# Optimization experiments

Measured on AMD Instinct MI355X. Metric: run time of the kernel, lower is better.

## Reference

```python
import jax, jax.numpy as jnp
import numpy as np

HID = 256

def lstm_cell(x, h, c, Wih, Whh, bih, bhh):
    # PyTorch LSTM gate order: i, f, g, o
    g = x @ Wih.T + h @ Whh.T + bih + bhh
    i, f, gg, o = jnp.split(g, 4, axis=-1)
    c = jax.nn.sigmoid(f) * c + jax.nn.sigmoid(i) * jnp.tanh(gg)
    h = jax.nn.sigmoid(o) * jnp.tanh(c)
    return h, c

def lstm_seq(x, Wih, Whh, bih, bhh):
    # x: [B, T, D] -> outputs [B, T, H], final (h, c)
    B = x.shape[0]
    h0 = jnp.zeros((B, HID), x.dtype)
    def step(carry, xt):
        h, c = lstm_cell(xt, carry[0], carry[1], Wih, Whh, bih, bhh)
        return (h, c), h
    (h, c), ys = jax.lax.scan(step, (h0, h0), jnp.swapaxes(x, 0, 1))
    return jnp.swapaxes(ys, 0, 1), h, c

def setup_inputs():
    key = jax.random.key(0)
    B, M, H_WIN, NTH, NTW = 512, 16, 25, 64, 64
    SAL = NTH * NTW
    ks = iter(jax.random.split(key, 40))
    def U(shape):
        return jax.random.uniform(next(ks), shape, jnp.float32, -0.0625, 0.0625)
    def lstm_p(pfx, din):
        return {pfx + '_Wih': U((4 * HID, din)), pfx + '_Whh': U((4 * HID, HID)),
                pfx + '_bih': U((4 * HID,)), pfx + '_bhh': U((4 * HID,))}
    inp = {
        'encoder_position_inputs': jax.random.normal(next(ks), (B, M, 3), jnp.float32) * 0.1,
        'encoder_saliency_inputs': jax.random.uniform(next(ks), (B, M, NTH, NTW), jnp.float32),
        'decoder_position_inputs': jax.random.normal(next(ks), (B, 1, 3), jnp.float32) * 0.1,
        'decoder_saliency_inputs': jax.random.uniform(next(ks), (B, H_WIN, NTH, NTW), jnp.float32),
    }
    for pfx, din in [('pe', 3), ('se', SAL), ('fe', 2 * HID), ('pd', 3), ('sd', SAL), ('fd', 2 * HID)]:
        inp.update(lstm_p(pfx, din))
    inp['f2_W'] = U((HID, HID)); inp['f2_b'] = U((HID,))
    inp['out_W'] = U((3, HID)); inp['out_b'] = U((3,))
    return inp

def reference(encoder_position_inputs, encoder_saliency_inputs, decoder_position_inputs, decoder_saliency_inputs,
              pe_Wih, pe_Whh, pe_bih, pe_bhh, se_Wih, se_Whh, se_bih, se_bhh,
              fe_Wih, fe_Whh, fe_bih, fe_bhh, pd_Wih, pd_Whh, pd_bih, pd_bhh,
              sd_Wih, sd_Whh, sd_bih, sd_bhh, fd_Wih, fd_Whh, fd_bih, fd_bhh,
              f2_W, f2_b, out_W, out_b):
    B, M = encoder_position_inputs.shape[:2]
    SAL = encoder_saliency_inputs.shape[2] * encoder_saliency_inputs.shape[3]
    # encoder
    out_pos, h1, c1 = lstm_seq(encoder_position_inputs, pe_Wih, pe_Whh, pe_bih, pe_bhh)
    out_sal, h2, c2 = lstm_seq(encoder_saliency_inputs.reshape(B, M, SAL), se_Wih, se_Whh, se_bih, se_bhh)
    conc_enc = jnp.concatenate([out_sal, out_pos], axis=-1)
    _, hf, cf = lstm_seq(conc_enc, fe_Wih, fe_Whh, fe_bih, fe_bhh)
    # decoder: H_WINDOW single-step recurrence; fuse LSTM restarts from (hf, cf) every step
    dec_sal = decoder_saliency_inputs.reshape(B, -1, SAL)
    def step(carry, sal_t):
        inp, h1, c1, h2, c2 = carry
        h1, c1 = lstm_cell(inp, h1, c1, pd_Wih, pd_Whh, pd_bih, pd_bhh)
        h2, c2 = lstm_cell(sal_t, h2, c2, sd_Wih, sd_Whh, sd_bih, sd_bhh)
        conc = jnp.concatenate([h2, h1], axis=-1)
        hfd, _ = lstm_cell(conc, hf, cf, fd_Wih, fd_Whh, fd_bih, fd_bhh)
        fuse2 = hfd @ f2_W.T + f2_b
        delta = fuse2 @ out_W.T + out_b
        pred = inp + delta  # toPosition: orientation + motion
        return (pred, h1, c1, h2, c2), pred
    init = (decoder_position_inputs[:, 0], h1, c1, h2, c2)
    _, preds = jax.lax.scan(step, init, jnp.swapaxes(dec_sal, 0, 1))
    return jnp.swapaxes(preds, 0, 1)  # [B, H_WINDOW, 3]
```

## Files before the change

kernel.cpp:

```cpp
#include <hip/hip_runtime.h>

#define HID 256
#define BATCH 512
#define MENC 16
#define HWIN 25
#define SALSZ 4096
#define BH (BATCH * HID)

typedef __attribute__((ext_vector_type(8))) short bf16x8;
typedef __attribute__((ext_vector_type(4))) float f32x4;

__device__ __forceinline__ float sigmf(float x) { return 1.0f / (1.0f + __expf(-x)); }
__device__ __forceinline__ ushort f2bf(float f) {
    uint32_t u = __float_as_uint(f);
    return (ushort)((u + 0x7fffu + ((u >> 16) & 1u)) >> 16);
}

#define GLOAD_LDS(gp, lp) \
    __builtin_amdgcn_global_load_lds((const __attribute__((address_space(1))) void*)(gp), \
                                     (__attribute__((address_space(3))) void*)(lp), 16, 0, 0)

__device__ __forceinline__ void st_u64(void* p, unsigned long long v) {
    __hip_atomic_store((unsigned long long*)p, v, __ATOMIC_RELAXED, __HIP_MEMORY_SCOPE_AGENT);
}
// ... 72 lines not shown
        const int row = idx >> 3, u = idx & 7;
        const int su = (u ^ (row & 7)) * 8;
        ra[2 * j + 0] = *(const float4*)(Ag + (size_t)row * lda + su);
        ra[2 * j + 1] = *(const float4*)(Ag + (size_t)row * lda + su + 4);
    }
}
__device__ __forceinline__ void writeA128(const float4 ra[4], ushort* Al, int tid)
{
#pragma unroll
    for (int j = 0; j < 2; ++j) {
        const int idx = j * 512 + tid;
        uint4 v;
        v.x = (uint)f2bf(ra[2 * j].x) | ((uint)f2bf(ra[2 * j].y) << 16);
        v.y = (uint)f2bf(ra[2 * j].z) | ((uint)f2bf(ra[2 * j].w) << 16);
        v.z = (uint)f2bf(ra[2 * j + 1].x) | ((uint)f2bf(ra[2 * j + 1].y) << 16);
        v.w = (uint)f2bf(ra[2 * j + 1].z) | ((uint)f2bf(ra[2 * j + 1].w) << 16);
        *(uint4*)(Al + idx * 8) = v;
    }
}
__device__ __forceinline__ void stageB128(const ushort* Bg, int ldw, ushort* Bl, int tid)
{
#pragma unroll
    for (int j = 0; j < 2; ++j) {
        const int idx = j * 512 + tid;
        const int row = idx >> 3, u = idx & 7;
        const int su = (u ^ (row & 7)) * 8;
        GLOAD_LDS(Bg + (size_t)row * ldw + su, Bl + idx * 8);
    }
}

__device__ __forceinline__ void gemm128f_body(
    const float* __restrict__ A, const ushort* __restrict__ W, float* __restrict__ C,
    int lda, int ldw, int ldc, int K, int gx, int nwg, int bid,
    ushort* AsB, ushort* BsB, int tid)
{
    const int lane = tid & 63, wid = tid >> 6;
    {
        const int q = nwg >> 3, r = nwg & 7;
        const int xcd = bid & 7, o = bid >> 3;
        bid = (xcd < r) ? xcd * (q + 1) + o : r * (q + 1) + (xcd - r) * q + o;
    }
    const int m0 = (bid / gx) * 128, n0 = (bid % gx) * 128;

    const int wr = wid >> 1, wc = wid & 1;
    const int fr = lane & 15, fq = lane >> 4;

    f32x4 acc[2][4] = {};
    const int nt = K / 64;
    const float*  Ab0 = A + (size_t)m0 * lda;
    const ushort* Bb0 = W + (size_t)n0 * ldw;

    float4 ra[4];
    loadA128(Ab0, lda, tid, ra);
    stageB128(Bb0, ldw, BsB, tid);
    writeA128(ra, AsB, tid);
    loadA128(Ab0 + 64, lda, tid, ra);
    asm volatile("s_waitcnt vmcnt(4) lgkmcnt(0)" ::: "memory");
    __builtin_amdgcn_sched_barrier(0);
    __builtin_amdgcn_s_barrier();
    __builtin_amdgcn_sched_barrier(0);

    for (int t = 0; t < nt; ++t) {
        const int p = t & 1;
        const int t1 = (t + 1 < nt) ? t + 1 : nt - 1;
        const int t2 = (t + 2 < nt) ? t + 2 : nt - 1;
        stageB128(Bb0 + t1 * 64, ldw, BsB + (p ^ 1) * 8192, tid);
// ... 8 lines not shown
#pragma unroll
            for (int nf = 0; nf < 4; ++nf) {
                const int row = wc * 64 + nf * 16 + fr;
                bfr[nf] = *(const bf16x8*)(Bb + row * 64 + ((ks * 4 + fq) ^ (row & 7)) * 8);
            }
            bf16x8 af[2];
#pragma unroll
            for (int mf = 0; mf < 2; ++mf) {
                const int row = wr * 32 + mf * 16 + fr;
                af[mf] = *(const bf16x8*)(Ab + row * 64 + ((ks * 4 + fq) ^ (row & 7)) * 8);
            }
            __builtin_amdgcn_s_setprio(1);
#pragma unroll
            for (int mf = 0; mf < 2; ++mf)
#pragma unroll
                for (int nf = 0; nf < 4; ++nf)
                    acc[mf][nf] = __builtin_amdgcn_mfma_f32_16x16x32_bf16(
                        af[mf], bfr[nf], acc[mf][nf], 0, 0, 0);
            __builtin_amdgcn_s_setprio(0);
        }
        if (t == nt - 1) break;
        asm volatile("s_waitcnt vmcnt(4) lgkmcnt(0)" ::: "memory");
        __builtin_amdgcn_sched_barrier(0);
        __builtin_amdgcn_s_barrier();
        __builtin_amdgcn_sched_barrier(0);
    }

    const int cl = lane & 15, ch = lane >> 4;
#pragma unroll
    for (int mf = 0; mf < 2; ++mf)
#pragma unroll
        for (int nf = 0; nf < 4; ++nf)
#pragma unroll
            for (int r = 0; r < 4; ++r)
                C[(size_t)(m0 + wr * 32 + mf * 16 + ch * 4 + r) * ldc
                  + n0 + wc * 64 + nf * 16 + cl] = acc[mf][nf][r];
}

__global__ __launch_bounds__(512, 4)
void gemm128f(const float* __restrict__ A, const ushort* __restrict__ W,
              float* __restrict__ C, int gx, int nwg)
{
    __shared__ ushort As[2 * 128 * 64];
    __shared__ ushort Bs[2 * 128 * 64];
    gemm128f_body(A, W, C, SALSZ, SALSZ, 1024, SALSZ, gx, nwg, blockIdx.x, As, Bs, threadIdx.x);
}

__device__ __forceinline__ void gemm128b_body(
    const ushort* __restrict__ A, const ushort* __restrict__ W, float* __restrict__ C,
    int lda, int ldw, int ldc, int K, int gx, int nwg, int bid,
    unsigned int* wflag, unsigned int wcnt, unsigned int* sflag, bool wt,
    ushort* AsB, ushort* BsB, int tid)
{
    const int lane = tid & 63, wid = tid >> 6;
    {
        const int q = nwg >> 3, r = nwg & 7;
        const int xcd = bid & 7, o = bid >> 3;
        bid = (xcd < r) ? xcd * (q + 1) + o : r * (q + 1) + (xcd - r) * q + o;
    }
    const int m0 = (bid / gx) * 128, n0 = (bid % gx) * 128;

    if (wflag) gbar_wait(wflag + (m0 >> 9), wcnt);

    const int wr = wid >> 1, wc = wid & 1;
    const int fr = lane & 15, fq = lane >> 4;

    f32x4 acc[2][4] = {};
    const int nt = K / 64;
    const ushort* Ab0 = A + (size_t)m0 * lda;
    const ushort* Bb0 = W + (size_t)n0 * ldw;

    stageB128(Ab0, lda, AsB, tid);
    stageB128(Bb0, ldw, BsB, tid);
    __syncthreads();

    for (int t = 0; t < nt; ++t) {
        const int p = t & 1;
        if (t + 1 < nt) {
            stageB128(Ab0 + (t + 1) * 64, lda, AsB + (p ^ 1) * 8192, tid);
            stageB128(Bb0 + (t + 1) * 64, ldw, BsB + (p ^ 1) * 8192, tid);
        }
        const ushort* Ab = AsB + p * 8192;
        const ushort* Bb = BsB + p * 8192;
#pragma unroll
        for (int ks = 0; ks < 2; ++ks) {
            bf16x8 bfr[4];
#pragma unroll
            for (int nf = 0; nf < 4; ++nf) {
                const int row = wc * 64 + nf * 16 + fr;
                bfr[nf] = *(const bf16x8*)(Bb + row * 64 + ((ks * 4 + fq) ^ (row & 7)) * 8);
            }
            bf16x8 af[2];
#pragma unroll
            for (int mf = 0; mf < 2; ++mf) {
                const int row = wr * 32 + mf * 16 + fr;
                af[mf] = *(const bf16x8*)(Ab + row * 64 + ((ks * 4 + fq) ^ (row & 7)) * 8);
            }
#pragma unroll
            for (int mf = 0; mf < 2; ++mf)
#pragma unroll
                for (int nf = 0; nf < 4; ++nf)
                    acc[mf][nf] = __builtin_amdgcn_mfma_f32_16x16x32_bf16(
                        af[mf], bfr[nf], acc[mf][nf], 0, 0, 0);
        }
        if (t == nt - 1) break;
        __syncthreads();
    }

    const int cl = lane & 15, ch = lane >> 4;
#pragma unroll
    for (int mf = 0; mf < 2; ++mf)
#pragma unroll
        for (int nf = 0; nf < 4; ++nf)
#pragma unroll
            for (int r = 0; r < 4; ++r) {
                const int mm = m0 + wr * 32 + mf * 16 + ch * 4 + r;
                const int nn = n0 + wc * 64 + nf * 16 + cl;
                if (wt) st_f32(C + (size_t)mm * ldc + nn, acc[mf][nf][r]);
                else    C[(size_t)mm * ldc + nn] = acc[mf][nf][r];
            }
    if (sflag) {
        __syncthreads();
        if (tid == 0) atomicAdd(sflag + (m0 >> 9), 1u);
    }
}

struct EncArgs {
    const ushort *WHse, *WHpe;
    const float  *xg_se;
    const float  *enc_pos;
    const float  *se_b1, *se_b2, *pe_b1, *pe_b2;
    const float  *pe_Wih;
    ushort       *conc;
    float        *SE_C, *PE_C;
    unsigned int *bar;
};

__global__ __launch_bounds__(512, 4)
void enc_sd(EncArgs A, const float* __restrict__ sdA, const ushort* __restrict__ sdW,
            float* __restrict__ sdC)
{
    __shared__ ushort sh[34816];
    const int tid = threadIdx.x;

    if (blockIdx.x >= 128) {
        gemm128f_body(sdA, sdW, sdC, SALSZ, SALSZ, 1024, SALSZ, 8, 800,
                      (int)blockIdx.x - 128, sh, sh + 16384, tid);
        return;
    }

    const int lane = tid & 63, w = tid >> 6;
    const int role  = blockIdx.x >> 6;
    const int rem   = blockIdx.x & 63;
    const int btile = rem & 7, usup = rem >> 3;
    const int b0 = btile * 64, ub = usup * 32;
    const int usub = w & 1, bsub = w >> 1;
    const int u0t = ub + usub * 16;
    const int grp = role * 8 + btile;
    const int fr = lane & 15, fq = lane >> 4;
    const int u = u0t + fr;
    const int ul = usub * 16 + fr;
    const int coff = role ? 256 : 0;
    ushort* Ws0 = sh + usub * 16384;
    ushort (*hloc)[32] = (ushort(*)[32])(sh + 32768);

    stage_wtile(role ? A.WHpe : A.WHse, HID, u0t, Ws0, lane, bsub);

    const float* b1 = role ? A.pe_b1 : A.se_b1;
    const float* b2 = role ? A.pe_b2 : A.se_b2;
    float bias[4], wxs[4][3];
#pragma unroll
    for (int g = 0; g < 4; ++g) {
        bias[g] = b1[g * HID + u] + b2[g * HID + u];
        wxs[g][0] = wxs[g][1] = wxs[g][2] = 0.0f;
        if (role) {
            wxs[g][0] = A.pe_Wih[(g * HID + u) * 3 + 0];
            wxs[g][1] = A.pe_Wih[(g * HID + u) * 3 + 1];
            wxs[g][2] = A.pe_Wih[(g * HID + u) * 3 + 2];
        }
    }
    float c[4] = {0.f, 0.f, 0.f, 0.f};
    __syncthreads();

    for (int t = 0; t < MENC; ++t) {
        float xg[4][4];
#pragma unroll
        for (int r = 0; r < 4; ++r) {
            const int b = b0 + bsub * 16 + fq * 4 + r;
            if (role) {
                const float* xp = A.enc_pos + ((size_t)b * MENC + t) * 3;
                xg[r][0] = xp[0]; xg[r][1] = xp[1]; xg[r][2] = xp[2]; xg[r][3] = 0.f;
            } else {
#pragma unroll
                for (int g = 0; g < 4; ++g)
                    xg[r][g] = A.xg_se[((size_t)b * MENC + t) * 1024 + g * HID + u];
            }
        }
        if (t > 0) gbar_wait(A.bar + grp * MENC + (t - 1), 8);
        f32x4 acc[4] = {};
        if (t > 0)
            cell_g(A.conc + ((size_t)(t - 1) * 512 + b0 + bsub * 16) * 512 + coff, 512,
                   Ws0, acc, lane);
#pragma unroll
        for (int r = 0; r < 4; ++r) {
            const int bl = bsub * 16 + fq * 4 + r;
            const int b = b0 + bl;
            float gv[4];
#pragma unroll
            for (int g = 0; g < 4; ++g) {
                float v = acc[g][r] + bias[g];
                if (role) v += xg[r][0] * wxs[g][0] + xg[r][1] * wxs[g][1] + xg[r][2] * wxs[g][2];
                else      v += xg[r][g];
                gv[g] = v;
            }
            const float cn = sigmf(gv[1]) * c[r] + sigmf(gv[0]) * tanhf(gv[2]);
            const float hn = sigmf(gv[3]) * tanhf(cn);
            c[r] = cn;
            hloc[bl][ul] = f2bf(hn);
            if (t == MENC - 1) (role ? A.PE_C : A.SE_C)[(size_t)b * HID + u] = cn;
        }
        __syncthreads();
        {
            const int row = tid >> 3, c8 = tid & 7;
            const unsigned long long v = *(const unsigned long long*)&hloc[row][c8 * 4];
            st_u64(A.conc + ((size_t)t * 512 + b0 + row) * 512 + coff + ub + c8 * 4, v);
        }
        if (t != MENC - 1) gbar_arrive(A.bar + grp * MENC + t);
    }
}

struct MidArgs {
    const ushort *WHsd, *WHfe;
    const float  *xg_sd;
    const float  *xg_fe;
    const float  *sd_b1, *sd_b2, *fe_b1, *fe_b2;
    const ushort *conc;
    const float  *SE_C;
    ushort       *SDB;
    ushort       *FEB;
    float        *FEH, *FE_C;
    unsigned int *bar;
    unsigned int *fe_done;
    unsigned int *sdb_done;
};

__global__ __launch_bounds__(512, 4)
void mid_fe_xh2(MidArgs A, const ushort* __restrict__ feA, const ushort* __restrict__ feW,
                float* __restrict__ feC,
                const ushort* __restrict__ xA, const ushort* __restrict__ xW,
                float* __restrict__ xC)
{
    __shared__ ushort sh[34816];
    const int tid = threadIdx.x;

    if (blockIdx.x >= 640) {
        gemm128b_body(xA, xW, xC, 256, 512, 1024, 256, 8, 800,
                      (int)blockIdx.x - 640, A.sdb_done, 64, nullptr, false,
                      sh, sh + 16384, tid);
        return;
    }
    if (blockIdx.x >= 128) {
        gemm128b_body(feA, feW, feC, 512, 512, 1024, 512, 8, 512,
                      (int)blockIdx.x - 128, nullptr, 0, A.fe_done, true,
                      sh, sh + 16384, tid);
        return;
    }

    const int lane = tid & 63, w = tid >> 6;
    const int role  = blockIdx.x >> 6;
    const int rem   = blockIdx.x & 63;
    const int btile = rem & 7, usup = rem >> 3;
    const int b0 = btile * 64, ub = usup * 32;
    const int usub = w & 1, bsub = w >> 1;
    const int u0t = ub + usub * 16;
    const int grp = role * 8 + btile;
    const int fr = lane & 15, fq = lane >> 4;
    const int u = u0t + fr;
    const int ul = usub * 16 + fr;
    const int NT = role ? MENC : HWIN;
    ushort* Ws0 = sh + usub * 16384;
    ushort (*hloc)[32] = (ushort(*)[32])(sh + 32768);

    stage_wtile(role ? A.WHfe : A.WHsd, HID, u0t, Ws0, lane, bsub);

    const float* b1 = role ? A.fe_b1 : A.sd_b1;
    const float* b2 = role ? A.fe_b2 : A.sd_b2;
    float bias[4];
#pragma unroll
    for (int g = 0; g < 4; ++g) bias[g] = b1[g * HID + u] + b2[g * HID + u];

    float c[4];
#pragma unroll
    for (int r = 0; r < 4; ++r) {
        const int b = b0 + bsub * 16 + fq * 4 + r;
        c[r] = role ? 0.0f : A.SE_C[(size_t)b * HID + u];
    }
    __syncthreads();

    for (int t = 0; t < NT; ++t) {
        if (role) gbar_wait(A.fe_done + t, 32);
        float xg[4][4];
#pragma unroll
        for (int r = 0; r < 4; ++r) {
            const int b = b0 + bsub * 16 + fq * 4 + r;
#pragma unroll
            for (int g = 0; g < 4; ++g)
                xg[r][g] = role ? A.xg_fe[((size_t)t * 512 + b) * 1024 + g * HID + u]
                                : A.xg_sd[((size_t)b * HWIN + t) * 1024 + g * HID + u];
        }
        if (t > 0) gbar_wait(A.bar + grp * HWIN + (t - 1), 8);
        f32x4 acc[4] = {};
        if (role == 0) {
            if (t == 0) cell_g(A.conc + ((size_t)15 * 512 + b0 + bsub * 16) * 512, 512,
                               Ws0, acc, lane);
            else        cell_g(A.SDB + ((size_t)(t - 1) * 512 + b0 + bsub * 16) * HID, HID,
                               Ws0, acc, lane);
        } else if (t > 0) {
            cell_g(A.FEB + ((size_t)(t - 1) * BATCH + b0 + bsub * 16) * HID, HID,
                   Ws0, acc, lane);
        }
#pragma unroll
        for (int r = 0; r < 4; ++r) {
            const int bl = bsub * 16 + fq * 4 + r;
            const int b = b0 + bl;
            float gv[4];
#pragma unroll
            for (int g = 0; g < 4; ++g)
                gv[g] = acc[g][r] + bias[g] + xg[r][g];
            const float cn = sigmf(gv[1]) * c[r] + sigmf(gv[0]) * tanhf(gv[2]);
            const float hn = sigmf(gv[3]) * tanhf(cn);
            c[r] = cn;
            hloc[bl][ul] = f2bf(hn);
            if (role == 1 && t == MENC - 1) {
                A.FEH[(size_t)b * HID + u] = hn;
                A.FE_C[(size_t)b * HID + u] = cn;
            }
        }
        __syncthreads();
        {
            const int row = tid >> 3, c8 = tid & 7;
            const unsigned long long v = *(const unsigned long long*)&hloc[row][c8 * 4];
            ushort* dst = role ? (A.FEB + ((size_t)t * BATCH + b0 + row) * 256 + ub + c8 * 4)
                               : (A.SDB + ((size_t)t * 512 + b0 + row) * 256 + ub + c8 * 4);
            st_u64(dst, v);
        }
        __syncthreads();
        if (tid == 0) {
            if (role == 0) atomicAdd(A.sdb_done + t, 1u);
            if (t != NT - 1) atomicAdd(A.bar + grp * HWIN + t, 1u);
        }
    }
}

__global__ __launch_bounds__(256)
void gemm_tn(const float* __restrict__ A, const float* __restrict__ W,
             const float* __restrict__ b1, const float* __restrict__ b2,
             float* __restrict__ C,
             int M, int N, int K, int lda, int ldw, int ldc)
{
    __shared__ float AsT[16][68];
    __shared__ float WsT[16][68];
    const int t  = threadIdx.x;
    const int tx = t & 15, ty = t >> 4;
    const int m0 = blockIdx.y * 64, n0 = blockIdx.x * 64;
    const int lr = t >> 2;
    const int c4 = t & 3;

    float acc[4][4];
#pragma unroll
    for (int i = 0; i < 4; ++i)
#pragma unroll
        for (int j = 0; j < 4; ++j) acc[i][j] = 0.0f;

    for (int k0 = 0; k0 < K; k0 += 16) {
        float a[4], w[4];
        const int kb = k0 + c4 * 4;
#pragma unroll
        for (int k = 0; k < 4; ++k) {
            a[k] = (kb + k < K) ? A[(size_t)(m0 + lr) * lda + kb + k] : 0.0f;
            w[k] = (kb + k < K) ? W[(size_t)(n0 + lr) * ldw + kb + k] : 0.0f;
        }
        __syncthreads();
#pragma unroll
        for (int k = 0; k < 4; ++k) {
            AsT[c4 * 4 + k][lr] = a[k];
            WsT[c4 * 4 + k][lr] = w[k];
        }
        __syncthreads();
#pragma unroll
        for (int kk = 0; kk < 16; ++kk) {
            const float4 av = *(const float4*)&AsT[kk][ty * 4];
            const float4 wv = *(const float4*)&WsT[kk][tx * 4];
            acc[0][0] += av.x * wv.x; acc[0][1] += av.x * wv.y; acc[0][2] += av.x * wv.z; acc[0][3] += av.x * wv.w;
            acc[1][0] += av.y * wv.x; acc[1][1] += av.y * wv.y; acc[1][2] += av.y * wv.z; acc[1][3] += av.y * wv.w;
            acc[2][0] += av.z * wv.x; acc[2][1] += av.z * wv.y; acc[2][2] += av.z * wv.z; acc[2][3] += av.z * wv.w;
            acc[3][0] += av.w * wv.x; acc[3][1] += av.w * wv.y; acc[3][2] += av.w * wv.z; acc[3][3] += av.w * wv.w;
        }
    }

#pragma unroll
    for (int i = 0; i < 4; ++i) {
        const int m = m0 + ty * 4 + i;
#pragma unroll
        for (int j = 0; j < 4; ++j) {
            const int n = n0 + tx * 4 + j;
            float v = acc[i][j];
            if (b1) v += b1[n];
            if (b2) v += b2[n];
            C[(size_t)m * ldc + n] = v;
        }
    }
}

struct DecArgs {
    const ushort *WHpd;
    const ushort *WFDh;
    const ushort *peF;
    const float  *PE_C, *FE_C, *GBIAS;
    const float  *xh2;
    const float  *pd_b1, *pd_b2, *pd_Wih;
    const float  *G, *c3, *dec_pos;
    ushort       *H1;
    float        *DELTA;
    float        *out;
    unsigned int *bar;
};

__global__ __launch_bounds__(512)
void dec_chain(DecArgs A)
{
    __shared__ ushort Wpd[2][64 * 256], Wfd[2][64 * 256];
    __shared__ ushort hloc[64][32];
    __shared__ float pred_lds[192];
    const int tid = threadIdx.x, lane = tid & 63, w = tid >> 6;
    const int btile = blockIdx.x & 7, usup = blockIdx.x >> 3;
    const int b0 = btile * 64, ub = usup * 32;
    const int usub = w & 1, bsub = w >> 1;
    const int u0t = ub + usub * 16;
    const int fr = lane & 15, fq = lane >> 4;
    const int u = u0t + fr;
    const int ul = usub * 16 + fr;
    unsigned int* bars = A.bar + btile * 2 * HWIN;

    stage_wtile(A.WHpd, HID, u0t, Wpd[usub], lane, bsub);
    stage_wtile(A.WFDh, 512, u0t, Wfd[usub], lane, bsub);

    float pdb[4], wxs[4][3], cf[4], c1[4], Gu[3], gb[4][4];
#pragma unroll
    for (int g = 0; g < 4; ++g) {
        pdb[g] = A.pd_b1[g * HID + u] + A.pd_b2[g * HID + u];
        wxs[g][0] = A.pd_Wih[(g * HID + u) * 3 + 0];
        wxs[g][1] = A.pd_Wih[(g * HID + u) * 3 + 1];
        wxs[g][2] = A.pd_Wih[(g * HID + u) * 3 + 2];
    }
#pragma unroll
    for (int r = 0; r < 4; ++r) {
        const int b = b0 + bsub * 16 + fq * 4 + r;
        c1[r] = A.PE_C[(size_t)b * HID + u];
        cf[r] = A.FE_C[(size_t)b * HID + u];
#pragma unroll
        for (int g = 0; g < 4; ++g) gb[r][g] = A.GBIAS[(size_t)b * 1024 + g * HID + u];
    }
    Gu[0] = A.G[0 * HID + u]; Gu[1] = A.G[1 * HID + u]; Gu[2] = A.G[2 * HID + u];
    const float c3r = (tid < 192) ? A.c3[tid % 3] : 0.0f;
    if (tid < 192) pred_lds[tid] = A.dec_pos[(size_t)(b0 + tid / 3) * 3 + tid % 3];
    __syncthreads();

    for (int t = 0; t < HWIN; ++t) {
        f32x4 acc[4] = {};
        if (t == 0) cell_g(A.peF + (size_t)(b0 + bsub * 16) * 512, 512, Wpd[usub], acc, lane);
        else        cell_g(A.H1 + ((size_t)(t - 1) * BATCH + b0 + bsub * 16) * HID, HID,
                           Wpd[usub], acc, lane);
        if (t > 0) {
            gbar_wait(bars + 2 * (t - 1) + 1, 8);
            if (tid < 192) {
                pred_lds[tid] += A.DELTA[((size_t)(t - 1) * 512 + b0 + tid / 3) * 3 + tid % 3] + c3r;
                if (usup == 0)
                    A.out[((size_t)(b0 + tid / 3) * HWIN + (t - 1)) * 3 + tid % 3] = pred_lds[tid];
            }
            __syncthreads();
        }
#pragma unroll
        for (int r = 0; r < 4; ++r) {
            const int bl = bsub * 16 + fq * 4 + r;
            const float x0 = pred_lds[bl * 3 + 0];
            const float x1 = pred_lds[bl * 3 + 1];
            const float x2 = pred_lds[bl * 3 + 2];
            float gv[4];
#pragma unroll
            for (int g = 0; g < 4; ++g)
                gv[g] = acc[g][r] + pdb[g] + x0 * wxs[g][0] + x1 * wxs[g][1] + x2 * wxs[g][2];
            const float cn = sigmf(gv[1]) * c1[r] + sigmf(gv[0]) * tanhf(gv[2]);
            const float hn = sigmf(gv[3]) * tanhf(cn);
            c1[r] = cn;
            hloc[bl][ul] = f2bf(hn);
        }
        __syncthreads();
        {
            const int row = tid >> 3, c8 = tid & 7;
            const unsigned long long v = *(const unsigned long long*)&hloc[row][c8 * 4];
            st_u64(A.H1 + ((size_t)t * BATCH + b0 + row) * 256 + ub + c8 * 4, v);
        }
        gbar_arrive(bars + 2 * t);
        float xh[4][4];
#pragma unroll
        for (int r = 0; r < 4; ++r) {
            const int b = b0 + bsub * 16 + fq * 4 + r;
#pragma unroll
            for (int g = 0; g < 4; ++g)
                xh[r][g] = A.xh2[((size_t)t * 512 + b) * 1024 + g * HID + u];
        }
        gbar_wait(bars + 2 * t, 8);
        {
            f32x4 accB[4] = {};
            cell_g(A.H1 + ((size_t)t * BATCH + b0 + bsub * 16) * HID, HID,
                   Wfd[usub], accB, lane);
#pragma unroll
            for (int r = 0; r < 4; ++r) {
                const int b = b0 + bsub * 16 + fq * 4 + r;
                float gv[4];
#pragma unroll
                for (int g = 0; g < 4; ++g)
                    gv[g] = accB[g][r] + xh[r][g] + gb[r][g];
                const float cn = sigmf(gv[1]) * cf[r] + sigmf(gv[0]) * tanhf(gv[2]);
                const float hn = sigmf(gv[3]) * tanhf(cn);
                float p0 = hn * Gu[0], p1 = hn * Gu[1], p2 = hn * Gu[2];
#pragma unroll
                for (int s = 1; s < 16; s <<= 1) {
                    p0 += __shfl_xor(p0, s);
                    p1 += __shfl_xor(p1, s);
                    p2 += __shfl_xor(p2, s);
                }
                if (fr == 0) {
                    float* d = A.DELTA + ((size_t)t * 512 + b) * 3;
                    atomicAdd(d + 0, p0); atomicAdd(d + 1, p1); atomicAdd(d + 2, p2);
                }
            }
        }
        gbar_arrive(bars + 2 * t + 1);
    }
    gbar_wait(bars + 2 * (HWIN - 1) + 1, 8);
    if (tid < 192) {
        pred_lds[tid] += A.DELTA[((size_t)(HWIN - 1) * 512 + b0 + tid / 3) * 3 + tid % 3] + c3r;
        if (usup == 0)
            A.out[((size_t)(b0 + tid / 3) * HWIN + (HWIN - 1)) * 3 + tid % 3] = pred_lds[tid];
    }
}

__global__ __launch_bounds__(256)
void precompute_G(const float* __restrict__ f2W, const float* __restrict__ f2b,
                  const float* __restrict__ outW, const float* __restrict__ outb,
                  float* __restrict__ G, float* __restrict__ c3)
{
    const int k = threadIdx.x;
    float g0 = 0.f, g1 = 0.f, g2 = 0.f;
    for (int n = 0; n < HID; ++n) {
        const float w = f2W[n * HID + k];
        g0 += outW[n] * w;
        g1 += outW[HID + n] * w;
        g2 += outW[2 * HID + n] * w;
    }
    G[k] = g0; G[HID + k] = g1; G[2 * HID + k] = g2;
    if (k < 3) {
        float s = outb[k];
        for (int n = 0; n < HID; ++n) s += outW[k * HID + n] * f2b[n];
        c3[k] = s;
    }
}

extern "C" void kernel_launch(void* const* d_in, const int* in_sizes, int n_in,
                              void* d_out, int out_size, void* d_ws, size_t ws_size,
                              hipStream_t stream)
{
    (void)in_sizes; (void)n_in; (void)out_size; (void)ws_size;
    const float* enc_pos = (const float*)d_in[0];
    const float* enc_sal = (const float*)d_in[1];
    const float* dec_pos = (const float*)d_in[2];
    const float* dec_sal = (const float*)d_in[3];
// ... 14 lines not shown
    float* out = (float*)d_out;
    float* ws  = (float*)d_ws;

    size_t off = 0;
    float* XG_SE = ws + off; off += (size_t)8192 * 1024;
    float* XG_FE = ws + off; off += (size_t)8192 * 1024;
    float* BIG   = ws + off; off += (size_t)12800 * 1024;
    float* BIG2  = ws + off; off += (size_t)12800 * 1024;
    float* GBIAS = ws + off; off += (size_t)BATCH * 1024;
    float* PE_C  = ws + off; off += BH;
    float* SE_C  = ws + off; off += BH;
    float* FE_C  = ws + off; off += BH;
    float* FEH   = ws + off; off += BH;
    float* Gm    = ws + off; off += 1024;
    float* C3    = ws + off; off += 8;
    float* DELTA = ws + off; off += (size_t)HWIN * BATCH * 3 + 64;
    unsigned int* BAR = (unsigned int*)(ws + off); off += 1280;
    ushort* WSE  = (ushort*)(ws + off); off += ((size_t)1024 * 4096) / 2;
    ushort* WSD  = (ushort*)(ws + off); off += ((size_t)1024 * 4096) / 2;
    ushort* WFE  = (ushort*)(ws + off); off += ((size_t)1024 * 512) / 2;
    ushort* WFD  = (ushort*)(ws + off); off += ((size_t)1024 * 512) / 2;
    ushort* WHpe = (ushort*)(ws + off); off += ((size_t)1024 * 256) / 2;
    ushort* WHse = (ushort*)(ws + off); off += ((size_t)1024 * 256) / 2;
    ushort* WHfe = (ushort*)(ws + off); off += ((size_t)1024 * 256) / 2;
    ushort* WHsd = (ushort*)(ws + off); off += ((size_t)1024 * 256) / 2;
    ushort* WHpd = (ushort*)(ws + off); off += ((size_t)1024 * 256) / 2;
    ushort* CONC = (ushort*)(ws + off); off += ((size_t)MENC * 512 * 512) / 2;
    ushort* SDB  = (ushort*)(ws + off); off += ((size_t)HWIN * BH) / 2;
    ushort* FEB  = (ushort*)(ws + off); off += ((size_t)MENC * BH) / 2;
    ushort* H1   = (ushort*)(ws + off); off += ((size_t)HWIN * BH) / 2;

    unsigned int* FE_DONE  = BAR + 1100;
    unsigned int* SDB_DONE = BAR + 1160;

    hipMemsetAsync(DELTA, 0, ((size_t)HWIN * BATCH * 3 + 64 + 1280) * 4, stream);

    {
        Cvt9 a;
        const float* srcs[9] = { se_Wih, sd_Wih, fe_Wih, fd_Wih, pe_Whh, se_Whh, fe_Whh, sd_Whh, pd_Whh };
        ushort*      dsts[9] = { WSE,    WSD,    WFE,    WFD,    WHpe,   WHse,   WHfe,   WHsd,   WHpd };
        const int    n4s[9]  = { 1024*4096/4, 1024*4096/4, 1024*512/4, 1024*512/4,
                                 1024*256/4, 1024*256/4, 1024*256/4, 1024*256/4, 1024*256/4 };
        int acc9 = 0;
        for (int i = 0; i < 9; ++i) { a.s[i] = srcs[i]; a.d[i] = dsts[i]; acc9 += n4s[i]; a.end[i] = acc9; }
        cvt_multi<<<(acc9 + 255) / 256, 256, 0, stream>>>(a);
    }
    precompute_G<<<1, 256, 0, stream>>>(f2_W, f2_b, out_W, out_b, Gm, C3);

    gemm128f<<<512, 512, 0, stream>>>(enc_sal, WSE, XG_SE, 8, 512);

    {
        EncArgs a;
        a.WHse = WHse; a.WHpe = WHpe; a.xg_se = XG_SE; a.enc_pos = enc_pos;
        a.se_b1 = se_bih; a.se_b2 = se_bhh; a.pe_b1 = pe_bih; a.pe_b2 = pe_bhh;
        a.pe_Wih = pe_Wih; a.conc = CONC; a.SE_C = SE_C; a.PE_C = PE_C;
        a.bar = BAR;
        enc_sd<<<928, 512, 0, stream>>>(a, dec_sal, WSD, BIG);
    }

    {
        MidArgs a;
        a.WHsd = WHsd; a.WHfe = WHfe; a.xg_sd = BIG; a.xg_fe = XG_FE;
        a.sd_b1 = sd_bih; a.sd_b2 = sd_bhh; a.fe_b1 = fe_bih; a.fe_b2 = fe_bhh;
        a.conc = CONC; a.SE_C = SE_C; a.SDB = SDB; a.FEB = FEB;
        a.FEH = FEH; a.FE_C = FE_C; a.bar = BAR + 256;
        a.fe_done = FE_DONE; a.sdb_done = SDB_DONE;
        mid_fe_xh2<<<1440, 512, 0, stream>>>(a, CONC, WFE, XG_FE, SDB, WFD, BIG2);
    }

    gemm_tn<<<dim3(16, 8), 256, 0, stream>>>(FEH, fd_Whh, fd_bih, fd_bhh, GBIAS,
                                             BATCH, 1024, HID, HID, HID, 1024);

    {
        DecArgs a;
        a.WHpd = WHpd; a.WFDh = WFD + 256;
        a.peF = CONC + ((size_t)15 * 512) * 512 + 256;
        a.PE_C = PE_C; a.FE_C = FE_C; a.GBIAS = GBIAS; a.xh2 = BIG2;
        a.pd_b1 = pd_bih; a.pd_b2 = pd_bhh; a.pd_Wih = pd_Wih;
        a.G = Gm; a.c3 = C3; a.dec_pos = dec_pos;
        a.H1 = H1; a.DELTA = DELTA; a.out = out; a.bar = BAR + 656;
        dec_chain<<<64, 512, 0, stream>>>(a);
    }
}
```

Measured before the change: 957.1 us.

## Merge mid-stage, bias GEMM and decoder chain into one persistent kernel

Folds the fd_Whh bias GEMM and the decoder recurrence into the mid-stage kernel as extra block roles, synchronised with global flag counters. The decoder can then start as soon as its inputs are ready instead of waiting at kernel boundaries. The xh2 GEMM now adds GBIAS in its epilogue, which removes the per-step bias add in the decoder. The decoder is re-tiled to 128-batch by 16-unit blocks. This removes two launches and lets the work overlap, but it relies on spin-wait barriers that assume all blocks are co-resident, and it changes the decoder's tile shape.

```diff
diff --git a/kernel.cpp b/kernel.cpp
--- a/kernel.cpp
+++ b/kernel.cpp
@@ -220,6 +220,7 @@
     const ushort* __restrict__ A, const ushort* __restrict__ W, float* __restrict__ C,
     int lda, int ldw, int ldc, int K, int gx, int nwg, int bid,
     unsigned int* wflag, unsigned int wcnt, unsigned int* sflag, bool wt,
+    const float* __restrict__ rbias,
     ushort* AsB, ushort* BsB, int tid)
 {
     const int lane = tid & 63, wid = tid >> 6;
@@ -286,8 +287,10 @@
             for (int r = 0; r < 4; ++r) {
                 const int mm = m0 + wr * 32 + mf * 16 + ch * 4 + r;
                 const int nn = n0 + wc * 64 + nf * 16 + cl;
-                if (wt) st_f32(C + (size_t)mm * ldc + nn, acc[mf][nf][r]);
-                else    C[(size_t)mm * ldc + nn] = acc[mf][nf][r];
+                float v = acc[mf][nf][r];
+                if (rbias) v += rbias[(size_t)(mm & 511) * ldc + nn];
+                if (wt) st_f32(C + (size_t)mm * ldc + nn, v);
+                else    C[(size_t)mm * ldc + nn] = v;
             }
     if (sflag) {
         __syncthreads();
@@ -399,10 +402,9 @@
     }
 }
 
-struct MidArgs {
+struct P3Args {
     const ushort *WHsd, *WHfe;
-    const float  *xg_sd;
-    const float  *xg_fe;
+    const float  *xg_sd, *xg_fe;
     const float  *sd_b1, *sd_b2, *fe_b1, *fe_b2;
     const ushort *conc;
     const float  *SE_C;
@@ -412,33 +414,208 @@
     unsigned int *bar;
     unsigned int *fe_done;
     unsigned int *sdb_done;
+    const ushort *feW;
+    float        *feC;
+    const float  *fd_Whh, *fd_b1, *fd_b2;
+    float        *GBIAS;
+    unsigned int *fe_fin;
+    unsigned int *gb_done;
+    const ushort *xW;
+    float        *xh2C;
+    unsigned int *xh2_done;
+    const ushort *WHpd, *WFDh, *peF;
+    const float  *PE_C;
+    const float  *pd_b1, *pd_b2, *pd_Wih;
+    const float  *G, *c3, *dec_pos;
+    ushort       *H1;
+    float        *DELTA;
+    float        *out;
+    unsigned int *dbar;
 };
 
+__device__ __forceinline__ void tn_body(const P3Args& A, int idx, ushort* shm, int tid)
+{
+    gbar_wait(A.fe_fin, 64);
+    float* As = (float*)shm;
+    float* Ws = As + 16 * 68;
+    const int m0 = (idx >> 4) * 64, n0 = (idx & 15) * 64;
+    const int lr = tid >> 3, kc = tid & 7;
+    const int tx = tid & 15, ty = tid >> 4;
+    float acc[2][4] = {};
+    for (int k0 = 0; k0 < HID; k0 += 16) {
+        const float a0 = A.FEH[(size_t)(m0 + lr) * HID + k0 + kc * 2];
+        const float a1 = A.FEH[(size_t)(m0 + lr) * HID + k0 + kc * 2 + 1];
+        const float w0 = A.fd_Whh[(size_t)(n0 + lr) * HID + k0 + kc * 2];
+        const float w1 = A.fd_Whh[(size_t)(n0 + lr) * HID + k0 + kc * 2 + 1];
+        __syncthreads();
+        As[(kc * 2) * 68 + lr] = a0; As[(kc * 2 + 1) * 68 + lr] = a1;
+        Ws[(kc * 2) * 68 + lr] = w0; Ws[(kc * 2 + 1) * 68 + lr] = w1;
+        __syncthreads();
+#pragma unroll
+        for (int kk = 0; kk < 16; ++kk) {
+            const float av0 = As[kk * 68 + ty * 2], av1 = As[kk * 68 + ty * 2 + 1];
+            const float4 wv = *(const float4*)&Ws[kk * 68 + tx * 4];
+            acc[0][0] += av0 * wv.x; acc[0][1] += av0 * wv.y; acc[0][2] += av0 * wv.z; acc[0][3] += av0 * wv.w;
+            acc[1][0] += av1 * wv.x; acc[1][1] += av1 * wv.y; acc[1][2] += av1 * wv.z; acc[1][3] += av1 * wv.w;
+        }
+    }
+#pragma unroll
+    for (int i = 0; i < 2; ++i) {
+        const int m = m0 + ty * 2 + i;
+#pragma unroll
+        for (int j = 0; j < 4; ++j) {
+            const int n = n0 + tx * 4 + j;
+            st_f32(A.GBIAS + (size_t)m * 1024 + n, acc[i][j] + A.fd_b1[n] + A.fd_b2[n]);
+        }
+    }
+    __syncthreads();
+    if (tid == 0) atomicAdd(A.gb_done, 1u);
+}
+
+__device__ __forceinline__ void dec_body(const P3Args& A, int idx, ushort* shm, int tid)
+{
+    ushort* Wpd = shm;
+    ushort* Wfd = shm + 16384;
+    ushort (*hloc)[16] = (ushort(*)[16])(shm + 32768);
+    float* pred_lds = (float*)(shm + 34816);
+    const int lane = tid & 63, w = tid >> 6;
+    const int btile = idx & 3, usup = idx >> 2;
+    const int b0 = btile * 128, u0t = usup * 16;
+    const int bsub = w;
+    const int fr = lane & 15, fq = lane >> 4;
+    const int u = u0t + fr;
+    unsigned int* bars = A.dbar + btile * 2 * HWIN;
+
+    if (w < 4) stage_wtile(A.WHpd, HID, u0t, Wpd, lane, w);
+    else       stage_wtile(A.WFDh, 512, u0t, Wfd, lane, w - 4);
+
+    float pdb[4], wxs[4][3], cf[4], c1[4], Gu[3];
+#pragma unroll
+    for (int g = 0; g < 4; ++g) {
+        pdb[g] = A.pd_b1[g * HID + u] + A.pd_b2[g * HID + u];
+        wxs[g][0] = A.pd_Wih[(g * HID + u) * 3 + 0];
+        wxs[g][1] = A.pd_Wih[(g * HID + u) * 3 + 1];
+        wxs[g][2] = A.pd_Wih[(g * HID + u) * 3 + 2];
+    }
+#pragma unroll
+    for (int r = 0; r < 4; ++r)
+        c1[r] = A.PE_C[(size_t)(b0 + bsub * 16 + fq * 4 + r) * HID + u];
+    Gu[0] = A.G[u]; Gu[1] = A.G[HID + u]; Gu[2] = A.G[2 * HID + u];
+    const float c3r = (tid < 384) ? A.c3[tid % 3] : 0.0f;
+    if (tid < 384) pred_lds[tid] = A.dec_pos[(size_t)(b0 + tid / 3) * 3 + tid % 3];
+
+    gbar_wait(A.gb_done, 128);
+#pragma unroll
+    for (int r = 0; r < 4; ++r)
+        cf[r] = A.FE_C[(size_t)(b0 + bsub * 16 + fq * 4 + r) * HID + u];
+
+    for (int t = 0; t < HWIN; ++t) {
+        f32x4 acc[4] = {};
+        if (t == 0) cell_g(A.peF + (size_t)(b0 + bsub * 16) * 512, 512, Wpd, acc, lane);
+        else        cell_g(A.H1 + ((size_t)(t - 1) * BATCH + b0 + bsub * 16) * HID, HID,
+                           Wpd, acc, lane);
+        if (t > 0) {
+            gbar_wait(bars + 2 * (t - 1) + 1, 16);
+            if (tid < 384) {
+                pred_lds[tid] += A.DELTA[((size_t)(t - 1) * 512 + b0 + tid / 3) * 3 + tid % 3] + c3r;
+                if (usup == 0)
+                    A.out[((size_t)(b0 + tid / 3) * HWIN + (t - 1)) * 3 + tid % 3] = pred_lds[tid];
+            }
+            __syncthreads();
+        }
+#pragma unroll
+        for (int r = 0; r < 4; ++r) {
+            const int bl = bsub * 16 + fq * 4 + r;
+            const float x0 = pred_lds[bl * 3 + 0];
+            const float x1 = pred_lds[bl * 3 + 1];
+            const float x2 = pred_lds[bl * 3 + 2];
+            float gv[4];
+#pragma unroll
+            for (int g = 0; g < 4; ++g)
+                gv[g] = acc[g][r] + pdb[g] + x0 * wxs[g][0] + x1 * wxs[g][1] + x2 * wxs[g][2];
+            const float cn = sigmf(gv[1]) * c1[r] + sigmf(gv[0]) * tanhf(gv[2]);
+            const float hn = sigmf(gv[3]) * tanhf(cn);
+            c1[r] = cn;
+            hloc[bl][fr] = f2bf(hn);
+        }
+        __syncthreads();
+        {
+            const int row = tid >> 2, c4 = tid & 3;
+            const unsigned long long v = *(const unsigned long long*)&hloc[row][c4 * 4];
+            st_u64(A.H1 + ((size_t)t * BATCH + b0 + row) * 256 + u0t + c4 * 4, v);
+        }
+        gbar_arrive(bars + 2 * t);
+        gbar_wait(A.xh2_done + t, 32);
+        float xh[4][4];
+#pragma unroll
+        for (int r = 0; r < 4; ++r) {
+            const int b = b0 + bsub * 16 + fq * 4 + r;
+#pragma unroll
+            for (int g = 0; g < 4; ++g)
+                xh[r][g] = A.xh2C[((size_t)t * 512 + b) * 1024 + g * HID + u];
+        }
+        gbar_wait(bars + 2 * t, 16);
+        {
+            f32x4 accB[4] = {};
+            cell_g(A.H1 + ((size_t)t * BATCH + b0 + bsub * 16) * HID, HID, Wfd, accB, lane);
+#pragma unroll
+            for (int r = 0; r < 4; ++r) {
+                const int b = b0 + bsub * 16 + fq * 4 + r;
+                float gv[4];
+#pragma unroll
+                for (int g = 0; g < 4; ++g)
+                    gv[g] = accB[g][r] + xh[r][g];
+                const float cn = sigmf(gv[1]) * cf[r] + sigmf(gv[0]) * tanhf(gv[2]);
+                const float hn = sigmf(gv[3]) * tanhf(cn);
+                float p0 = hn * Gu[0], p1 = hn * Gu[1], p2 = hn * Gu[2];
+#pragma unroll
+                for (int s = 1; s < 16; s <<= 1) {
+                    p0 += __shfl_xor(p0, s);
+                    p1 += __shfl_xor(p1, s);
+                    p2 += __shfl_xor(p2, s);
+                }
+                if (fr == 0) {
+                    float* d = A.DELTA + ((size_t)t * 512 + b) * 3;
+                    atomicAdd(d + 0, p0); atomicAdd(d + 1, p1); atomicAdd(d + 2, p2);
+                }
+            }
+        }
+        gbar_arrive(bars + 2 * t + 1);
+    }
+    gbar_wait(bars + 2 * (HWIN - 1) + 1, 16);
+    if (tid < 384) {
+        pred_lds[tid] += A.DELTA[((size_t)(HWIN - 1) * 512 + b0 + tid / 3) * 3 + tid % 3] + c3r;
+        if (usup == 0)
+            A.out[((size_t)(b0 + tid / 3) * HWIN + (HWIN - 1)) * 3 + tid % 3] = pred_lds[tid];
+    }
+}
+
 __global__ __launch_bounds__(512, 4)
-void mid_fe_xh2(MidArgs A, const ushort* __restrict__ feA, const ushort* __restrict__ feW,
-                float* __restrict__ feC,
-                const ushort* __restrict__ xA, const ushort* __restrict__ xW,
-                float* __restrict__ xC)
-{
-    __shared__ ushort sh[34816];
+void mid_dec(P3Args A)
+{
+    __shared__ ushort sh[35584];
     const int tid = threadIdx.x;
-
-    if (blockIdx.x >= 640) {
-        gemm128b_body(xA, xW, xC, 256, 512, 1024, 256, 8, 800,
-                      (int)blockIdx.x - 640, A.sdb_done, 64, nullptr, false,
+    const int blk = (int)blockIdx.x;
+
+    if (blk >= 832) {
+        gbar_wait(A.gb_done, 128);
+        gemm128b_body(A.SDB, A.xW, A.xh2C, 256, 512, 1024, 256, 8, 800,
+                      blk - 832, A.sdb_done, 64, A.xh2_done, true, A.GBIAS,
                       sh, sh + 16384, tid);
         return;
     }
-    if (blockIdx.x >= 128) {
-        gemm128b_body(feA, feW, feC, 512, 512, 1024, 512, 8, 512,
-                      (int)blockIdx.x - 128, nullptr, 0, A.fe_done, true,
+    if (blk >= 768) { dec_body(A, blk - 768, sh, tid); return; }
+    if (blk >= 640) { tn_body(A, blk - 640, sh, tid); return; }
+    if (blk >= 128) {
+        gemm128b_body(A.conc, A.feW, A.feC, 512, 512, 1024, 512, 8, 512,
+                      blk - 128, nullptr, 0, A.fe_done, true, nullptr,
                       sh, sh + 16384, tid);
         return;
     }
 
     const int lane = tid & 63, w = tid >> 6;
-    const int role  = blockIdx.x >> 6;
-    const int rem   = blockIdx.x & 63;
+    const int role  = blk >> 6;
+    const int rem   = blk & 63;
     const int btile = rem & 7, usup = rem >> 3;
     const int b0 = btile * 64, ub = usup * 32;
     const int usub = w & 1, bsub = w >> 1;
@@ -502,8 +679,8 @@
             c[r] = cn;
             hloc[bl][ul] = f2bf(hn);
             if (role == 1 && t == MENC - 1) {
-                A.FEH[(size_t)b * HID + u] = hn;
-                A.FE_C[(size_t)b * HID + u] = cn;
+                st_f32(A.FEH + (size_t)b * HID + u, hn);
+                st_f32(A.FE_C + (size_t)b * HID + u, cn);
             }
         }
         __syncthreads();
@@ -520,200 +697,8 @@
             if (t != NT - 1) atomicAdd(A.bar + grp * HWIN + t, 1u);
         }
     }
-}
-
-__global__ __launch_bounds__(256)
-void gemm_tn(const float* __restrict__ A, const float* __restrict__ W,
-             const float* __restrict__ b1, const float* __restrict__ b2,
-             float* __restrict__ C,
-             int M, int N, int K, int lda, int ldw, int ldc)
-{
-    __shared__ float AsT[16][68];
-    __shared__ float WsT[16][68];
-    const int t  = threadIdx.x;
-    const int tx = t & 15, ty = t >> 4;
-    const int m0 = blockIdx.y * 64, n0 = blockIdx.x * 64;
-    const int lr = t >> 2;
-    const int c4 = t & 3;
-
-    float acc[4][4];
-#pragma unroll
-    for (int i = 0; i < 4; ++i)
-#pragma unroll
-        for (int j = 0; j < 4; ++j) acc[i][j] = 0.0f;
-
-    for (int k0 = 0; k0 < K; k0 += 16) {
-        float a[4], w[4];
-        const int kb = k0 + c4 * 4;
-#pragma unroll
-        for (int k = 0; k < 4; ++k) {
-            a[k] = (kb + k < K) ? A[(size_t)(m0 + lr) * lda + kb + k] : 0.0f;
-            w[k] = (kb + k < K) ? W[(size_t)(n0 + lr) * ldw + kb + k] : 0.0f;
-        }
-        __syncthreads();
-#pragma unroll
-        for (int k = 0; k < 4; ++k) {
-            AsT[c4 * 4 + k][lr] = a[k];
-            WsT[c4 * 4 + k][lr] = w[k];
-        }
-        __syncthreads();
-#pragma unroll
-        for (int kk = 0; kk < 16; ++kk) {
-            const float4 av = *(const float4*)&AsT[kk][ty * 4];
-            const float4 wv = *(const float4*)&WsT[kk][tx * 4];
-            acc[0][0] += av.x * wv.x; acc[0][1] += av.x * wv.y; acc[0][2] += av.x * wv.z; acc[0][3] += av.x * wv.w;
-            acc[1][0] += av.y * wv.x; acc[1][1] += av.y * wv.y; acc[1][2] += av.y * wv.z; acc[1][3] += av.y * wv.w;
-            acc[2][0] += av.z * wv.x; acc[2][1] += av.z * wv.y; acc[2][2] += av.z * wv.z; acc[2][3] += av.z * wv.w;
-            acc[3][0] += av.w * wv.x; acc[3][1] += av.w * wv.y; acc[3][2] += av.w * wv.z; acc[3][3] += av.w * wv.w;
-        }
-    }
-
-#pragma unroll
-    for (int i = 0; i < 4; ++i) {
-        const int m = m0 + ty * 4 + i;
-#pragma unroll
-        for (int j = 0; j < 4; ++j) {
-            const int n = n0 + tx * 4 + j;
-            float v = acc[i][j];
-            if (b1) v += b1[n];
-            if (b2) v += b2[n];
-            C[(size_t)m * ldc + n] = v;
-        }
-    }
-}
-
-struct DecArgs {
-    const ushort *WHpd;
-    const ushort *WFDh;
-    const ushort *peF;
-    const float  *PE_C, *FE_C, *GBIAS;
-    const float  *xh2;
-    const float  *pd_b1, *pd_b2, *pd_Wih;
-    const float  *G, *c3, *dec_pos;
-    ushort       *H1;
-    float        *DELTA;
-    float        *out;
-    unsigned int *bar;
-};
-
-__global__ __launch_bounds__(512)
-void dec_chain(DecArgs A)
-{
-    __shared__ ushort Wpd[2][64 * 256], Wfd[2][64 * 256];
-    __shared__ ushort hloc[64][32];
-    __shared__ float pred_lds[192];
-    const int tid = threadIdx.x, lane = tid & 63, w = tid >> 6;
-    const int btile = blockIdx.x & 7, usup = blockIdx.x >> 3;
-    const int b0 = btile * 64, ub = usup * 32;
-    const int usub = w & 1, bsub = w >> 1;
-    const int u0t = ub + usub * 16;
-    const int fr = lane & 15, fq = lane >> 4;
-    const int u = u0t + fr;
-    const int ul = usub * 16 + fr;
-    unsigned int* bars = A.bar + btile * 2 * HWIN;
-
-    stage_wtile(A.WHpd, HID, u0t, Wpd[usub], lane, bsub);
-    stage_wtile(A.WFDh, 512, u0t, Wfd[usub], lane, bsub);
-
-    float pdb[4], wxs[4][3], cf[4], c1[4], Gu[3], gb[4][4];
-#pragma unroll
-    for (int g = 0; g < 4; ++g) {
-        pdb[g] = A.pd_b1[g * HID + u] + A.pd_b2[g * HID + u];
-        wxs[g][0] = A.pd_Wih[(g * HID + u) * 3 + 0];
-        wxs[g][1] = A.pd_Wih[(g * HID + u) * 3 + 1];
-        wxs[g][2] = A.pd_Wih[(g * HID + u) * 3 + 2];
-    }
-#pragma unroll
-    for (int r = 0; r < 4; ++r) {
-        const int b = b0 + bsub * 16 + fq * 4 + r;
-        c1[r] = A.PE_C[(size_t)b * HID + u];
-        cf[r] = A.FE_C[(size_t)b * HID + u];
-#pragma unroll
-        for (int g = 0; g < 4; ++g) gb[r][g] = A.GBIAS[(size_t)b * 1024 + g * HID + u];
-    }
-    Gu[0] = A.G[0 * HID + u]; Gu[1] = A.G[1 * HID + u]; Gu[2] = A.G[2 * HID + u];
-    const float c3r = (tid < 192) ? A.c3[tid % 3] : 0.0f;
-    if (tid < 192) pred_lds[tid] = A.dec_pos[(size_t)(b0 + tid / 3) * 3 + tid % 3];
-    __syncthreads();
-
-    for (int t = 0; t < HWIN; ++t) {
-        f32x4 acc[4] = {};
-        if (t == 0) cell_g(A.peF + (size_t)(b0 + bsub * 16) * 512, 512, Wpd[usub], acc, lane);
-        else        cell_g(A.H1 + ((size_t)(t - 1) * BATCH + b0 + bsub * 16) * HID, HID,
-                           Wpd[usub], acc, lane);
-        if (t > 0) {
-            gbar_wait(bars + 2 * (t - 1) + 1, 8);
-            if (tid < 192) {
-                pred_lds[tid] += A.DELTA[((size_t)(t - 1) * 512 + b0 + tid / 3) * 3 + tid % 3] + c3r;
-                if (usup == 0)
-                    A.out[((size_t)(b0 + tid / 3) * HWIN + (t - 1)) * 3 + tid % 3] = pred_lds[tid];
-            }
-            __syncthreads();
-        }
-#pragma unroll
-        for (int r = 0; r < 4; ++r) {
-            const int bl = bsub * 16 + fq * 4 + r;
-            const float x0 = pred_lds[bl * 3 + 0];
-            const float x1 = pred_lds[bl * 3 + 1];
-            const float x2 = pred_lds[bl * 3 + 2];
-            float gv[4];
-#pragma unroll
-            for (int g = 0; g < 4; ++g)
-                gv[g] = acc[g][r] + pdb[g] + x0 * wxs[g][0] + x1 * wxs[g][1] + x2 * wxs[g][2];
-            const float cn = sigmf(gv[1]) * c1[r] + sigmf(gv[0]) * tanhf(gv[2]);
-            const float hn = sigmf(gv[3]) * tanhf(cn);
-            c1[r] = cn;
-            hloc[bl][ul] = f2bf(hn);
-        }
-        __syncthreads();
-        {
-            const int row = tid >> 3, c8 = tid & 7;
-            const unsigned long long v = *(const unsigned long long*)&hloc[row][c8 * 4];
-            st_u64(A.H1 + ((size_t)t * BATCH + b0 + row) * 256 + ub + c8 * 4, v);
-        }
-        gbar_arrive(bars + 2 * t);
-        float xh[4][4];
-#pragma unroll
-        for (int r = 0; r < 4; ++r) {
-            const int b = b0 + bsub * 16 + fq * 4 + r;
-#pragma unroll
-            for (int g = 0; g < 4; ++g)
-                xh[r][g] = A.xh2[((size_t)t * 512 + b) * 1024 + g * HID + u];
-        }
-        gbar_wait(bars + 2 * t, 8);
-        {
-            f32x4 accB[4] = {};
-            cell_g(A.H1 + ((size_t)t * BATCH + b0 + bsub * 16) * HID, HID,
-                   Wfd[usub], accB, lane);
-#pragma unroll
-            for (int r = 0; r < 4; ++r) {
-                const int b = b0 + bsub * 16 + fq * 4 + r;
-                float gv[4];
-#pragma unroll
-                for (int g = 0; g < 4; ++g)
-                    gv[g] = accB[g][r] + xh[r][g] + gb[r][g];
-                const float cn = sigmf(gv[1]) * cf[r] + sigmf(gv[0]) * tanhf(gv[2]);
-                const float hn = sigmf(gv[3]) * tanhf(cn);
-                float p0 = hn * Gu[0], p1 = hn * Gu[1], p2 = hn * Gu[2];
-#pragma unroll
-                for (int s = 1; s < 16; s <<= 1) {
-                    p0 += __shfl_xor(p0, s);
-                    p1 += __shfl_xor(p1, s);
-                    p2 += __shfl_xor(p2, s);
-                }
-                if (fr == 0) {
-                    float* d = A.DELTA + ((size_t)t * 512 + b) * 3;
-                    atomicAdd(d + 0, p0); atomicAdd(d + 1, p1); atomicAdd(d + 2, p2);
-                }
-            }
-        }
-        gbar_arrive(bars + 2 * t + 1);
-    }
-    gbar_wait(bars + 2 * (HWIN - 1) + 1, 8);
-    if (tid < 192) {
-        pred_lds[tid] += A.DELTA[((size_t)(HWIN - 1) * 512 + b0 + tid / 3) * 3 + tid % 3] + c3r;
-        if (usup == 0)
-            A.out[((size_t)(b0 + tid / 3) * HWIN + (HWIN - 1)) * 3 + tid % 3] = pred_lds[tid];
+    if (role == 1) {
+        if (tid == 0) atomicAdd(A.fe_fin, 1u);
     }
 }
 
@@ -794,6 +779,9 @@
 
     unsigned int* FE_DONE  = BAR + 1100;
     unsigned int* SDB_DONE = BAR + 1160;
+    unsigned int* FE_FIN   = BAR + 1200;
+    unsigned int* GB_DONE  = BAR + 1204;
+    unsigned int* XH2_DONE = BAR + 1220;
 
     hipMemsetAsync(DELTA, 0, ((size_t)HWIN * BATCH * 3 + 64 + 1280) * 4, stream);
 
@@ -821,26 +809,22 @@
     }
 
     {
-        MidArgs a;
+        P3Args a;
         a.WHsd = WHsd; a.WHfe = WHfe; a.xg_sd = BIG; a.xg_fe = XG_FE;
         a.sd_b1 = sd_bih; a.sd_b2 = sd_bhh; a.fe_b1 = fe_bih; a.fe_b2 = fe_bhh;
         a.conc = CONC; a.SE_C = SE_C; a.SDB = SDB; a.FEB = FEB;
-        a.FEH = FEH; a.FE_C = FE_C; a.bar = BAR + 256;
-        a.fe_done = FE_DONE; a.sdb_done = SDB_DONE;
-        mid_fe_xh2<<<1440, 512, 0, stream>>>(a, CONC, WFE, XG_FE, SDB, WFD, BIG2);
-    }
-
-    gemm_tn<<<dim3(16, 8), 256, 0, stream>>>(FEH, fd_Whh, fd_bih, fd_bhh, GBIAS,
-                                             BATCH, 1024, HID, HID, HID, 1024);
-
-    {
-        DecArgs a;
+        a.FEH = FEH; a.FE_C = FE_C;
+        a.bar = BAR + 256; a.fe_done = FE_DONE; a.sdb_done = SDB_DONE;
+        a.feW = WFE; a.feC = XG_FE;
+        a.fd_Whh = fd_Whh; a.fd_b1 = fd_bih; a.fd_b2 = fd_bhh; a.GBIAS = GBIAS;
+        a.fe_fin = FE_FIN; a.gb_done = GB_DONE;
+        a.xW = WFD; a.xh2C = BIG2; a.xh2_done = XH2_DONE;
         a.WHpd = WHpd; a.WFDh = WFD + 256;
         a.peF = CONC + ((size_t)15 * 512) * 512 + 256;
-        a.PE_C = PE_C; a.FE_C = FE_C; a.GBIAS = GBIAS; a.xh2 = BIG2;
+        a.PE_C = PE_C;
         a.pd_b1 = pd_bih; a.pd_b2 = pd_bhh; a.pd_Wih = pd_Wih;
         a.G = Gm; a.c3 = C3; a.dec_pos = dec_pos;
-        a.H1 = H1; a.DELTA = DELTA; a.out = out; a.bar = BAR + 656;
-        dec_chain<<<64, 512, 0, stream>>>(a);
-    }
-}
+        a.H1 = H1; a.DELTA = DELTA; a.out = out; a.dbar = BAR + 656;
+        mid_dec<<<1632, 512, 0, stream>>>(a);
+    }
+}
```

After: 974.3 us. About the same (+1.8%).

## Fuse encoder saliency input GEMM into enc_sd kernel with per-tile completion flags

Applied to the files above, without the earlier changes.

Removes the standalone gemm128f launch for the encoder saliency input projection and runs it as extra workgroups inside enc_sd. Each GEMM tile publishes completion through per-batch-tile atomic counters (SE_DONE), and the saliency recurrence groups spin-wait on their batch tile's counter before starting. This overlaps the position LSTM and decoder-saliency GEMM with the encoder GEMM and drops a kernel boundary. In exchange it adds spin-wait and release/acquire costs, and it depends on the GEMM workgroups being scheduled while the recurrence blocks spin, which carries a deadlock risk.

```diff
diff --git a/kernel.cpp b/kernel.cpp
--- a/kernel.cpp
+++ b/kernel.cpp
@@ -128,6 +128,7 @@
 __device__ __forceinline__ void gemm128f_body(
     const float* __restrict__ A, const ushort* __restrict__ W, float* __restrict__ C,
     int lda, int ldw, int ldc, int K, int gx, int nwg, int bid,
+    unsigned int* sflag, bool wt,
     ushort* AsB, ushort* BsB, int tid)
 {
     const int lane = tid & 63, wid = tid >> 6;
@@ -202,18 +203,16 @@
 #pragma unroll
         for (int nf = 0; nf < 4; ++nf)
 #pragma unroll
-            for (int r = 0; r < 4; ++r)
-                C[(size_t)(m0 + wr * 32 + mf * 16 + ch * 4 + r) * ldc
-                  + n0 + wc * 64 + nf * 16 + cl] = acc[mf][nf][r];
-}
-
-__global__ __launch_bounds__(512, 4)
-void gemm128f(const float* __restrict__ A, const ushort* __restrict__ W,
-              float* __restrict__ C, int gx, int nwg)
-{
-    __shared__ ushort As[2 * 128 * 64];
-    __shared__ ushort Bs[2 * 128 * 64];
-    gemm128f_body(A, W, C, SALSZ, SALSZ, 1024, SALSZ, gx, nwg, blockIdx.x, As, Bs, threadIdx.x);
+            for (int r = 0; r < 4; ++r) {
+                const int mm = m0 + wr * 32 + mf * 16 + ch * 4 + r;
+                const int nn = n0 + wc * 64 + nf * 16 + cl;
+                if (wt) st_f32(C + (size_t)mm * ldc + nn, acc[mf][nf][r]);
+                else    C[(size_t)mm * ldc + nn] = acc[mf][nf][r];
+            }
+    if (sflag) {
+        __syncthreads();
+        if (tid == 0) atomicAdd(sflag + (m0 >> 10), 1u);
+    }
 }
 
 __device__ __forceinline__ void gemm128b_body(
@@ -304,18 +303,26 @@
     ushort       *conc;
     float        *SE_C, *PE_C;
     unsigned int *bar;
+    unsigned int *se_done;
 };
 
 __global__ __launch_bounds__(512, 4)
-void enc_sd(EncArgs A, const float* __restrict__ sdA, const ushort* __restrict__ sdW,
+void enc_sd(EncArgs A, const float* __restrict__ seA, const ushort* __restrict__ seW,
+            float* __restrict__ seC,
+            const float* __restrict__ sdA, const ushort* __restrict__ sdW,
             float* __restrict__ sdC)
 {
     __shared__ ushort sh[34816];
     const int tid = threadIdx.x;
 
+    if (blockIdx.x >= 640) {
+        gemm128f_body(sdA, sdW, sdC, SALSZ, SALSZ, 1024, SALSZ, 8, 800,
+                      (int)blockIdx.x - 640, nullptr, false, sh, sh + 16384, tid);
+        return;
+    }
     if (blockIdx.x >= 128) {
-        gemm128f_body(sdA, sdW, sdC, SALSZ, SALSZ, 1024, SALSZ, 8, 800,
-                      (int)blockIdx.x - 128, sh, sh + 16384, tid);
+        gemm128f_body(seA, seW, seC, SALSZ, SALSZ, 1024, SALSZ, 8, 512,
+                      (int)blockIdx.x - 128, A.se_done, true, sh, sh + 16384, tid);
         return;
     }
 
@@ -351,6 +358,8 @@
     }
     float c[4] = {0.f, 0.f, 0.f, 0.f};
     __syncthreads();
+
+    if (!role) gbar_wait(A.se_done + btile, 64);
 
     for (int t = 0; t < MENC; ++t) {
         float xg[4][4];
@@ -794,6 +803,7 @@
 
     unsigned int* FE_DONE  = BAR + 1100;
     unsigned int* SDB_DONE = BAR + 1160;
+    unsigned int* SE_DONE  = BAR + 1240;
 
     hipMemsetAsync(DELTA, 0, ((size_t)HWIN * BATCH * 3 + 64 + 1280) * 4, stream);
 
@@ -809,15 +819,13 @@
     }
     precompute_G<<<1, 256, 0, stream>>>(f2_W, f2_b, out_W, out_b, Gm, C3);
 
-    gemm128f<<<512, 512, 0, stream>>>(enc_sal, WSE, XG_SE, 8, 512);
-
     {
         EncArgs a;
         a.WHse = WHse; a.WHpe = WHpe; a.xg_se = XG_SE; a.enc_pos = enc_pos;
         a.se_b1 = se_bih; a.se_b2 = se_bhh; a.pe_b1 = pe_bih; a.pe_b2 = pe_bhh;
         a.pe_Wih = pe_Wih; a.conc = CONC; a.SE_C = SE_C; a.PE_C = PE_C;
-        a.bar = BAR;
-        enc_sd<<<928, 512, 0, stream>>>(a, dec_sal, WSD, BIG);
+        a.bar = BAR; a.se_done = SE_DONE;
+        enc_sd<<<1440, 512, 0, stream>>>(a, enc_sal, WSE, XG_SE, dec_sal, WSD, BIG);
     }
 
     {
```

New measurement: 993.2 us. 1.04x slower.
